# Kernel tuning notes

Hardware: AMD Instinct MI355X
Metric: run time of the kernel (lower is better)

Reference implementation:

```python
import jax, jax.numpy as jnp
import numpy as np

B, N, D, H = 16, 512, 512, 8
DK = D // H
SCALE = DK ** (-0.5)
NEG = -9.0e15
LN_EPS = 1e-5


def setup_inputs() -> dict:
    key = jax.random.key(0)
    ks = jax.random.split(key, 16)
    std = 1.0 / np.sqrt(D)
    x = jax.random.normal(ks[0], (B, N, D), jnp.float32)
    adj = jax.random.randint(ks[1], (B, N, N), 0, 2).astype(jnp.float32)
    # weights stored [in, out] (y = x @ W + b)
    def lin(k, fin, fout):
        return jax.random.normal(k, (fin, fout), jnp.float32) * (1.0 / np.sqrt(fin))
    return {
        "x": x,
        "adj": adj,
        "W_w": lin(ks[2], D, D), "W_b": jnp.zeros((D,), jnp.float32),
        "ln_g": jnp.ones((D,), jnp.float32), "ln_b": jnp.zeros((D,), jnp.float32),
        "Wq": lin(ks[3], D, D), "bq": jnp.zeros((D,), jnp.float32),
        "Wk": lin(ks[4], D, D), "bk": jnp.zeros((D,), jnp.float32),
        "Wv": lin(ks[5], D, D), "bv": jnp.zeros((D,), jnp.float32),
        "Wo": lin(ks[6], D, D), "bo": jnp.zeros((D,), jnp.float32),
        "gate_w": lin(ks[7], 2 * D, 1), "gate_b": jnp.zeros((1,), jnp.float32),
        "use_adj": 1,
    }


def _layernorm(h, g, b):
    mu = jnp.mean(h, axis=-1, keepdims=True)
    var = jnp.mean(jnp.square(h - mu), axis=-1, keepdims=True)
    return (h - mu) * jax.lax.rsqrt(var + LN_EPS) * g + b


def _forward(x, adj, W_w, W_b, ln_g, ln_b, Wq, bq, Wk, bk, Wv, bv, Wo, bo, gate_w, gate_b, use_adj):
    h = x @ W_w + W_b                      # [B,N,D]
    h = _layernorm(h, ln_g, ln_b)
    q = (h @ Wq + bq).reshape(B, N, H, DK)
    k = (h @ Wk + bk).reshape(B, N, H, DK)
    v = (h @ Wv + bv).reshape(B, N, H, DK)
    scores = jnp.einsum('bqhd,bkhd->bhqk', q * SCALE, k)   # [B,H,N,N]
    if use_adj:
        a = adj[:, None, :, :]
        scores = jnp.where(a > 0, scores, NEG) * a
    attn = jax.nn.softmax(scores, axis=-1)
    ctx = jnp.einsum('bhqk,bkhd->bqhd', attn, v).reshape(B, N, D)
    h2 = jax.nn.relu(ctx @ Wo + bo)        # dropout = identity (eval)
    coeff = jax.nn.sigmoid(jnp.concatenate([x, h2], axis=-1) @ gate_w + gate_b)  # [B,N,1]
    return coeff * x + (1.0 - coeff) * h2


def reference(x, adj, W_w, W_b, ln_g, ln_b, Wq, bq, Wk, bk, Wv, bv, Wo, bo, gate_w, gate_b, use_adj):
    return _forward(x, adj, W_w, W_b, ln_g, ln_b, Wq, bq, Wk, bk, Wv, bv, Wo, bo, gate_w, gate_b, use_adj)
```

## Files before the change

kernel.cpp:

```cpp
#include <hip/hip_runtime.h>
#include <stdint.h>


typedef __bf16 bf16_t;
typedef __bf16 bf16x8 __attribute__((ext_vector_type(8)));
typedef float  f32x4  __attribute__((ext_vector_type(4)));

#define B_   16
#define N_   512
#define D_   512
#define H_   8
#define DK_  64
#define BN_  8192
#define LOG2E 1.4426950408889634f

__device__ __forceinline__ void gl2lds16(const void* g, void* l) {
  __builtin_amdgcn_global_load_lds(
      (const __attribute__((address_space(1))) void*)g,
      (__attribute__((address_space(3))) void*)l, 16, 0, 0);
}

struct WPrep { const float* src[5]; bf16_t* dst[5]; };
__global__ __launch_bounds__(256) void k_prep(const float* __restrict__ x,
                                              bf16_t* __restrict__ xb,
                                              WPrep p) {
  __shared__ float tile[32][33];
  const int blk = blockIdx.x;
  const int t = threadIdx.x;
  if (blk < 2048) {
    const long i = ((long)blk * 256 + t) * 8;
    float4 a = *(const float4*)&x[i];
    float4 b = *(const float4*)&x[i + 4];
    bf16x8 o;
    o[0] = (bf16_t)a.x; o[1] = (bf16_t)a.y; o[2] = (bf16_t)a.z; o[3] = (bf16_t)a.w;
    o[4] = (bf16_t)b.x; o[5] = (bf16_t)b.y; o[6] = (bf16_t)b.z; o[7] = (bf16_t)b.w;
    *(bf16x8*)&xb[i] = o;
  } else {
    const int r = blk - 2048;
    const int z = r >> 8, rem = r & 255;
    const float* W = p.src[z];
    bf16_t* Wt = p.dst[z];
    const int kb = (rem & 15) * 32, nb = (rem >> 4) * 32;
    const int tx = t & 31, ty = t >> 5;
#pragma unroll
    for (int i = ty; i < 32; i += 8)
      tile[i][tx] = W[(long)(kb + i) * D_ + nb + tx];
    __syncthreads();
#pragma unroll
    for (int i = ty; i < 32; i += 8)
      Wt[(long)(nb + i) * D_ + kb + tx] = (bf16_t)tile[tx][i];
  }
}

template <int OMODE, int TN>
__global__ __launch_bounds__(256) void k_gemm128(const bf16_t* __restrict__ A,
                                                 const bf16_t* __restrict__ Bt,
                                                 const float* __restrict__ b0,
                                                 const float* __restrict__ b1,
                                                 const float* __restrict__ b2,
                                                 float s0, float s1, float s2,
                                                 void* __restrict__ outp, int ldOut,
                                                 bf16_t* __restrict__ vtp) {
  constexpr int MI = (TN == 128) ? 4 : 2;
  __shared__ bf16_t As[2][128 * 32];
  __shared__ bf16_t Bs[2][TN * 32];
  const int t = threadIdx.x;
  const int m0 = blockIdx.x * 128;
  const int n0 = blockIdx.y * TN;
  const int w = t >> 6, lane = t & 63;
  const int quad = lane >> 4, l16 = lane & 15;
  const int wm = (TN == 128) ? (w >> 1) * 64 : w * 32;
  const int wn = (TN == 128) ? (w & 1) * 64 : 0;

  const int e0 = t * 8;
  const int r0 = e0 >> 5, c0 = e0 & 31;
  const bf16_t* agp0 = A + (long)(m0 + r0) * 512 + c0;
  const bf16_t* agp1 = agp0 + (long)64 * 512;
  const bf16_t* bgp0 = Bt + (long)(n0 + r0) * 512 + c0;
  const bf16_t* bgp1 = bgp0 + (long)64 * 512;

  f32x4 acc[MI][4] = {};

  gl2lds16(agp0, &As[0][e0]);
  gl2lds16(agp1, &As[0][e0 + 2048]);
  gl2lds16(bgp0, &Bs[0][e0]);
  if (TN == 128) gl2lds16(bgp1, &Bs[0][e0 + 2048]);
  __syncthreads();

  int cur = 0;
  for (int k0 = 0; k0 < 512; k0 += 32) {
    const int nxt = cur ^ 1;
    if (k0 + 32 < 512) {
      gl2lds16(agp0 + k0 + 32, &As[nxt][e0]);
      gl2lds16(agp1 + k0 + 32, &As[nxt][e0 + 2048]);
      gl2lds16(bgp0 + k0 + 32, &Bs[nxt][e0]);
      if (TN == 128) gl2lds16(bgp1 + k0 + 32, &Bs[nxt][e0 + 2048]);
    }

    bf16x8 af[MI], bfr[4];
#pragma unroll
    for (int i = 0; i < MI; ++i)
      af[i]  = *(const bf16x8*)&As[cur][(wm + i * 16 + l16) * 32 + quad * 8];
#pragma unroll
    for (int i = 0; i < 4; ++i)
      bfr[i] = *(const bf16x8*)&Bs[cur][(wn + i * 16 + l16) * 32 + quad * 8];
#pragma unroll
    for (int mi = 0; mi < MI; ++mi)
#pragma unroll
      for (int ni = 0; ni < 4; ++ni)
        acc[mi][ni] = __builtin_amdgcn_mfma_f32_16x16x32_bf16(af[mi], bfr[ni],
                                                              acc[mi][ni], 0, 0, 0);
    __syncthreads();
    cur = nxt;
  }

  const int seg = n0 >> 9;
  const float* bias = (seg == 0) ? b0 : (seg == 1) ? b1 : b2;
  const float scale = (seg == 0) ? s0 : (seg == 1) ? s1 : s2;
#pragma unroll
  for (int ni = 0; ni < 4; ++ni) {
    const int n = n0 + wn + ni * 16 + l16;
    const float bv = bias[n & 511];
#pragma unroll
    for (int mi = 0; mi < MI; ++mi)
#pragma unroll
      for (int r = 0; r < 4; ++r) {
        const long m = m0 + wm + mi * 16 + quad * 4 + r;
        float v = (acc[mi][ni][r] + bv) * scale;
        if (OMODE == 2) v = fmaxf(v, 0.0f);
        if (OMODE == 3) {
          if (seg < 2) {
            ((bf16_t*)outp)[m * 1024 + n] = (bf16_t)v;
          } else {
            const int tok = (int)m & 511, bb = (int)(m >> 9);
            const int hh = (n >> 6) & 7, dk = n & 63;
            vtp[(((long)bb * 8 + hh) * 64 + dk) * 512 + tok] = (bf16_t)v;
          }
        } else {
          ((float*)outp)[m * ldOut + n] = v;
        }
      }
  }
}

__global__ __launch_bounds__(256) void k_layernorm(const float* __restrict__ hp,
                                                   const float* __restrict__ g,
                                                   const float* __restrict__ bb,
                                                   bf16_t* __restrict__ out) {
  const int row = blockIdx.x * 4 + (threadIdx.x >> 6);
  const int lane = threadIdx.x & 63;
  const float* hr = hp + (long)row * D_;
  float v[8];
  *(float4*)&v[0] = ((const float4*)hr)[lane * 2];
  *(float4*)&v[4] = ((const float4*)hr)[lane * 2 + 1];
  float s = 0.f;
#pragma unroll
  for (int i = 0; i < 8; ++i) s += v[i];
#pragma unroll
  for (int o = 32; o > 0; o >>= 1) s += __shfl_xor(s, o, 64);
  const float mu = s * (1.0f / 512.0f);
  float vs = 0.f;
#pragma unroll
  for (int i = 0; i < 8; ++i) { float d = v[i] - mu; vs += d * d; }
#pragma unroll
  for (int o = 32; o > 0; o >>= 1) vs += __shfl_xor(vs, o, 64);
  const float rstd = rsqrtf(vs * (1.0f / 512.0f) + 1e-5f);
  float gv[8], bv[8];
  *(float4*)&gv[0] = ((const float4*)g)[lane * 2];
  *(float4*)&gv[4] = ((const float4*)g)[lane * 2 + 1];
  *(float4*)&bv[0] = ((const float4*)bb)[lane * 2];
  *(float4*)&bv[4] = ((const float4*)bb)[lane * 2 + 1];
  bf16x8 o8;
#pragma unroll
  for (int i = 0; i < 8; ++i) o8[i] = (bf16_t)((v[i] - mu) * rstd * gv[i] + bv[i]);
  *(bf16x8*)&out[(long)row * D_ + lane * 8] = o8;
}

__global__ __launch_bounds__(256) void k_attn(const bf16_t* __restrict__ qk,
                                              const bf16_t* __restrict__ vT,
                                              const float* __restrict__ adj,
                                              const int* __restrict__ use_adj_p,
                                              bf16_t* __restrict__ ctx) {
  __shared__ bf16_t Ks[64][72];
  __shared__ bf16_t Vs[64][72];
  __shared__ bf16_t Ps[4][16][72];
  const int t = threadIdx.x;
  const int w = t >> 6, lane = t & 63;
  const int quad = lane >> 4, l16 = lane & 15;
  const int bh = blockIdx.x & 127;
  const int qt = blockIdx.x >> 7;
  const int b = bh >> 3, h = bh & 7;
  const int q0 = qt * 64;
  const int use_adj = use_adj_p[0];

  const long qoff = (long)(b * N_ + q0 + w * 16 + l16) * 1024 + h * DK_ + quad * 8;
  const bf16x8 aq0 = *(const bf16x8*)&qk[qoff];
  const bf16x8 aq1 = *(const bf16x8*)&qk[qoff + 32];

  const int sr = t >> 2, sc = (t & 3) * 16;
  const bf16_t* kbase  = qk + (long)b * N_ * 1024 + 512 + h * DK_;
  const bf16_t* vtbase = vT + (long)bh * DK_ * N_;
  const float*  abase  = adj + ((long)b * N_ + q0 + w * 16 + quad * 4) * N_;

  f32x4 accO[4] = {};
  float l_part[4] = {0.f, 0.f, 0.f, 0.f};

  for (int kt = 0; kt < 8; ++kt) {
    __syncthreads();
    {
      const bf16_t* ksrc = kbase + (long)(kt * 64 + sr) * 1024 + sc;
      *(uint4*)&Ks[sr][sc]     = *(const uint4*)ksrc;
      *(uint4*)&Ks[sr][sc + 8] = *(const uint4*)(ksrc + 8);
      const bf16_t* vsrc = vtbase + (long)sr * N_ + kt * 64 + sc;
      *(uint4*)&Vs[sr][sc]     = *(const uint4*)vsrc;
      *(uint4*)&Vs[sr][sc + 8] = *(const uint4*)(vsrc + 8);
    }
    __syncthreads();

    f32x4 s[4];
#pragma unroll
    for (int nt = 0; nt < 4; ++nt) {
      bf16x8 bk0 = *(const bf16x8*)&Ks[nt * 16 + l16][quad * 8];
      bf16x8 bk1 = *(const bf16x8*)&Ks[nt * 16 + l16][quad * 8 + 32];
      f32x4 z = {};
      z = __builtin_amdgcn_mfma_f32_16x16x32_bf16(aq0, bk0, z, 0, 0, 0);
      z = __builtin_amdgcn_mfma_f32_16x16x32_bf16(aq1, bk1, z, 0, 0, 0);
      s[nt] = z;
    }

    if (use_adj) {
#pragma unroll
      for (int nt = 0; nt < 4; ++nt)
#pragma unroll
        for (int r = 0; r < 4; ++r)
          s[nt][r] *= abase[(long)r * N_ + kt * 64 + nt * 16 + l16];
    }

#pragma unroll
    for (int nt = 0; nt < 4; ++nt)
#pragma unroll
      for (int r = 0; r < 4; ++r) {
        const float e = __builtin_amdgcn_exp2f(s[nt][r]);
        s[nt][r] = e;
        l_part[r] += e;
      }

#pragma unroll
    for (int nt = 0; nt < 4; ++nt)
#pragma unroll
      for (int r = 0; r < 4; ++r)
        Ps[w][quad * 4 + r][nt * 16 + l16] = (bf16_t)s[nt][r];
    __builtin_amdgcn_s_waitcnt(0xC07F);

    bf16x8 ap0 = *(const bf16x8*)&Ps[w][l16][quad * 8];
    bf16x8 ap1 = *(const bf16x8*)&Ps[w][l16][quad * 8 + 32];
#pragma unroll
    for (int nt = 0; nt < 4; ++nt) {
      bf16x8 bv0 = *(const bf16x8*)&Vs[nt * 16 + l16][quad * 8];
      bf16x8 bv1 = *(const bf16x8*)&Vs[nt * 16 + l16][quad * 8 + 32];
      accO[nt] = __builtin_amdgcn_mfma_f32_16x16x32_bf16(ap0, bv0, accO[nt], 0, 0, 0);
      accO[nt] = __builtin_amdgcn_mfma_f32_16x16x32_bf16(ap1, bv1, accO[nt], 0, 0, 0);
    }
  }

#pragma unroll
  for (int o = 1; o < 16; o <<= 1)
#pragma unroll
    for (int r = 0; r < 4; ++r) l_part[r] += __shfl_xor(l_part[r], o, 64);
  float inv[4];
#pragma unroll
  for (int r = 0; r < 4; ++r) inv[r] = 1.0f / l_part[r];
#pragma unroll
  for (int r = 0; r < 4; ++r) {
    const long orow = (long)(b * N_ + q0 + w * 16 + quad * 4 + r) * D_ + h * DK_;
#pragma unroll
    for (int nt = 0; nt < 4; ++nt)
      ctx[orow + nt * 16 + l16] = (bf16_t)(accO[nt][r] * inv[r]);
  }
}

__global__ __launch_bounds__(256) void k_gate(const float* __restrict__ x,
                                              const float* __restrict__ h2,
                                              const float* __restrict__ gw,
                                              const float* __restrict__ gb,
                                              float* __restrict__ outp) {
  const int row = blockIdx.x * 4 + (threadIdx.x >> 6);
  const int lane = threadIdx.x & 63;
  const long base = (long)row * D_ + lane * 8;
  float xv[8], hv[8], w0[8], w1[8];
  *(float4*)&xv[0] = *(const float4*)&x[base];
  *(float4*)&xv[4] = *(const float4*)&x[base + 4];
  *(float4*)&hv[0] = *(const float4*)&h2[base];
  *(float4*)&hv[4] = *(const float4*)&h2[base + 4];
  *(float4*)&w0[0] = *(const float4*)&gw[lane * 8];
  *(float4*)&w0[4] = *(const float4*)&gw[lane * 8 + 4];
  *(float4*)&w1[0] = *(const float4*)&gw[512 + lane * 8];
  *(float4*)&w1[4] = *(const float4*)&gw[512 + lane * 8 + 4];
  float s = 0.f;
#pragma unroll
  for (int i = 0; i < 8; ++i) s += xv[i] * w0[i] + hv[i] * w1[i];
#pragma unroll
  for (int o = 32; o > 0; o >>= 1) s += __shfl_xor(s, o, 64);
  const float z = s + gb[0];
  const float coeff = 1.0f / (1.0f + __expf(-z));
#pragma unroll
  for (int i = 0; i < 8; ++i)
    outp[base + i] = coeff * xv[i] + (1.0f - coeff) * hv[i];
}

extern "C" void kernel_launch(void* const* d_in, const int* in_sizes, int n_in,
                              void* d_out, int out_size, void* d_ws, size_t ws_size,
                              hipStream_t stream) {
  (void)in_sizes; (void)n_in; (void)out_size; (void)ws_size;
  const float* x    = (const float*)d_in[0];
  const float* adj  = (const float*)d_in[1];
  const float* W_w  = (const float*)d_in[2];
  const float* W_b  = (const float*)d_in[3];
  const float* ln_g = (const float*)d_in[4];
  const float* ln_b = (const float*)d_in[5];
  const float* Wq   = (const float*)d_in[6];
  const float* bq   = (const float*)d_in[7];
  const float* Wk   = (const float*)d_in[8];
  const float* bk   = (const float*)d_in[9];
  const float* Wv   = (const float*)d_in[10];
  const float* bv   = (const float*)d_in[11];
  const float* Wo   = (const float*)d_in[12];
  const float* bo   = (const float*)d_in[13];
  const float* gw   = (const float*)d_in[14];
  const float* gb   = (const float*)d_in[15];
  const int* use_adj = (const int*)d_in[16];

  char* ws = (char*)d_ws;
  size_t off = 0;
  auto alloc = [&](size_t bytes) -> void* {
    void* p = ws + off;
    off += (bytes + 255) & ~(size_t)255;
    return p;
  };
  bf16_t*  WtW   = (bf16_t*)alloc((size_t)D_ * D_ * 2);
  bf16_t*  WtQKV = (bf16_t*)alloc((size_t)3 * D_ * D_ * 2);
  bf16_t*  WtO   = (bf16_t*)alloc((size_t)D_ * D_ * 2);
  bf16_t*  xb    = (bf16_t*)alloc((size_t)BN_ * D_ * 2);
  float*   hPre  = (float*)alloc((size_t)BN_ * D_ * 4);
  bf16_t*  hB    = (bf16_t*)alloc((size_t)BN_ * D_ * 2);
  bf16_t*  qkB   = (bf16_t*)alloc((size_t)BN_ * 2 * D_ * 2);
  bf16_t*  vTB   = (bf16_t*)alloc((size_t)BN_ * D_ * 2);
  bf16_t*  ctxB  = (bf16_t*)alloc((size_t)BN_ * D_ * 2);
  float*   h2    = hPre;

  WPrep wp;
  wp.src[0] = W_w; wp.dst[0] = WtW;
  wp.src[1] = Wq;  wp.dst[1] = WtQKV;
  wp.src[2] = Wk;  wp.dst[2] = WtQKV + (size_t)D_ * D_;
  wp.src[3] = Wv;  wp.dst[3] = WtQKV + (size_t)2 * D_ * D_;
  wp.src[4] = Wo;  wp.dst[4] = WtO;
  k_prep<<<3328, 256, 0, stream>>>(x, xb, wp);

  dim3 gh(BN_ / 128, D_ / 64);
  dim3 gqkv(BN_ / 128, 3 * D_ / 128);
  k_gemm128<0, 64><<<gh, 256, 0, stream>>>(xb, WtW, W_b, W_b, W_b, 1.f, 1.f, 1.f,
                                           hPre, D_, nullptr);
  k_layernorm<<<BN_ / 4, 256, 0, stream>>>(hPre, ln_g, ln_b, hB);
  k_gemm128<3, 128><<<gqkv, 256, 0, stream>>>(hB, WtQKV, bq, bk, bv,
                                              0.125f * LOG2E, 1.f, 1.f, qkB, 1024, vTB);
  k_attn<<<1024, 256, 0, stream>>>(qkB, vTB, adj, use_adj, ctxB);
  k_gemm128<2, 64><<<gh, 256, 0, stream>>>(ctxB, WtO, bo, bo, bo, 1.f, 1.f, 1.f,
                                           h2, D_, nullptr);
  k_gate<<<BN_ / 4, 256, 0, stream>>>(x, h2, gw, gb, (float*)d_out);
}
```

Measured before the change: 202.7 us.

## Fuse layernorm and gate into full-row GEMM epilogues

Adds a full-row GEMM kernel in which each 512-thread block computes 32 complete output rows, so row reductions can be done in the epilogue. The first GEMM now applies layernorm directly and writes bf16, which removes the fp32 hPre round trip and the separate layernorm launch. The output-projection GEMM computes ReLU, the sigmoid gate and the blend in its epilogue, which removes the h2 buffer and the gate launch. In exchange, each block streams the whole 512x512 weight matrix through a large LDS buffer, occupancy may drop, and variance is now computed in one pass as E[x^2]-mu^2.

```diff
diff --git a/kernel.cpp b/kernel.cpp
--- a/kernel.cpp
+++ b/kernel.cpp
@@ -52,25 +52,199 @@
   }
 }
 
-template <int OMODE, int TN>
-__global__ __launch_bounds__(256) void k_gemm128(const bf16_t* __restrict__ A,
-                                                 const bf16_t* __restrict__ Bt,
-                                                 const float* __restrict__ b0,
-                                                 const float* __restrict__ b1,
-                                                 const float* __restrict__ b2,
-                                                 float s0, float s1, float s2,
-                                                 void* __restrict__ outp, int ldOut,
-                                                 bf16_t* __restrict__ vtp) {
-  constexpr int MI = (TN == 128) ? 4 : 2;
+template <int MODE>
+__global__ __launch_bounds__(512) void k_gemm_row(const bf16_t* __restrict__ A,
+                                                  const bf16_t* __restrict__ Bt,
+                                                  const float* __restrict__ bias,
+                                                  const float* __restrict__ p0,
+                                                  const float* __restrict__ p1,
+                                                  const float* __restrict__ p2,
+                                                  void* __restrict__ outp) {
+  __shared__ bf16_t As[2][32 * 32];
+  __shared__ bf16_t Bs[2][512 * 32];
+  __shared__ float red[8][32][2];
+  __shared__ float rowc[32][2];
+  const int t = threadIdx.x;
+  const int w = t >> 6, lane = t & 63;
+  const int quad = lane >> 4, l16 = lane & 15;
+  const int m0 = blockIdx.x * 32;
+  const int wn = w * 64;
+
+  const int ea = t * 8;
+  const bf16_t* agp = A + (long)(m0 + (ea >> 5)) * 512 + (ea & 31);
+  const bf16_t* bgp[4];
+  int eb[4];
+#pragma unroll
+  for (int j = 0; j < 4; ++j) {
+    eb[j] = j * 4096 + t * 8;
+    bgp[j] = Bt + (long)(eb[j] >> 5) * 512 + (eb[j] & 31);
+  }
+
+  f32x4 acc[2][4] = {};
+
+  if (t < 128) gl2lds16(agp, &As[0][ea]);
+#pragma unroll
+  for (int j = 0; j < 4; ++j) gl2lds16(bgp[j], &Bs[0][eb[j]]);
+  __syncthreads();
+
+  int cur = 0;
+  for (int k0 = 0; k0 < 512; k0 += 32) {
+    const int nxt = cur ^ 1;
+    if (k0 + 32 < 512) {
+      if (t < 128) gl2lds16(agp + k0 + 32, &As[nxt][ea]);
+#pragma unroll
+      for (int j = 0; j < 4; ++j) gl2lds16(bgp[j] + k0 + 32, &Bs[nxt][eb[j]]);
+    }
+    bf16x8 af[2], bfr[4];
+#pragma unroll
+    for (int mi = 0; mi < 2; ++mi)
+      af[mi] = *(const bf16x8*)&As[cur][(mi * 16 + l16) * 32 + quad * 8];
+#pragma unroll
+    for (int ni = 0; ni < 4; ++ni)
+      bfr[ni] = *(const bf16x8*)&Bs[cur][(wn + ni * 16 + l16) * 32 + quad * 8];
+#pragma unroll
+    for (int mi = 0; mi < 2; ++mi)
+#pragma unroll
+      for (int ni = 0; ni < 4; ++ni)
+        acc[mi][ni] = __builtin_amdgcn_mfma_f32_16x16x32_bf16(af[mi], bfr[ni],
+                                                              acc[mi][ni], 0, 0, 0);
+    __syncthreads();
+    cur = nxt;
+  }
+
+  float bv[4];
+#pragma unroll
+  for (int ni = 0; ni < 4; ++ni) bv[ni] = bias[wn + ni * 16 + l16];
+
+  if (MODE == 0) {
+#pragma unroll
+    for (int mi = 0; mi < 2; ++mi)
+#pragma unroll
+      for (int r = 0; r < 4; ++r) {
+        float s1 = 0.f, s2 = 0.f;
+#pragma unroll
+        for (int ni = 0; ni < 4; ++ni) {
+          const float v = acc[mi][ni][r] + bv[ni];
+          s1 += v; s2 += v * v;
+        }
+#pragma unroll
+        for (int o = 1; o < 16; o <<= 1) {
+          s1 += __shfl_xor(s1, o, 64);
+          s2 += __shfl_xor(s2, o, 64);
+        }
+        if (l16 == 0) {
+          const int row = mi * 16 + quad * 4 + r;
+          red[w][row][0] = s1; red[w][row][1] = s2;
+        }
+      }
+    __syncthreads();
+    if (t < 32) {
+      float S1 = 0.f, S2 = 0.f;
+#pragma unroll
+      for (int wv = 0; wv < 8; ++wv) { S1 += red[wv][t][0]; S2 += red[wv][t][1]; }
+      const float mu = S1 * (1.0f / 512.0f);
+      const float var = S2 * (1.0f / 512.0f) - mu * mu;
+      rowc[t][0] = mu;
+      rowc[t][1] = rsqrtf(var + 1e-5f);
+    }
+    __syncthreads();
+    float gv[4], b2[4];
+#pragma unroll
+    for (int ni = 0; ni < 4; ++ni) {
+      gv[ni] = p0[wn + ni * 16 + l16];
+      b2[ni] = p1[wn + ni * 16 + l16];
+    }
+#pragma unroll
+    for (int mi = 0; mi < 2; ++mi)
+#pragma unroll
+      for (int r = 0; r < 4; ++r) {
+        const int row = mi * 16 + quad * 4 + r;
+        const float mu = rowc[row][0], rs = rowc[row][1];
+#pragma unroll
+        for (int ni = 0; ni < 4; ++ni) {
+          const float v = acc[mi][ni][r] + bv[ni];
+          ((bf16_t*)outp)[(long)(m0 + row) * 512 + wn + ni * 16 + l16] =
+              (bf16_t)((v - mu) * rs * gv[ni] + b2[ni]);
+        }
+      }
+  } else {
+    float g0[4], g1[4];
+#pragma unroll
+    for (int ni = 0; ni < 4; ++ni) {
+      g0[ni] = p1[wn + ni * 16 + l16];
+      g1[ni] = p1[512 + wn + ni * 16 + l16];
+    }
+    float xr[2][4][4];
+#pragma unroll
+    for (int mi = 0; mi < 2; ++mi)
+#pragma unroll
+      for (int r = 0; r < 4; ++r) {
+        const int row = mi * 16 + quad * 4 + r;
+#pragma unroll
+        for (int ni = 0; ni < 4; ++ni)
+          xr[mi][ni][r] = p0[(long)(m0 + row) * 512 + wn + ni * 16 + l16];
+      }
+#pragma unroll
+    for (int mi = 0; mi < 2; ++mi)
+#pragma unroll
+      for (int r = 0; r < 4; ++r) {
+        float px = 0.f, ph = 0.f;
+#pragma unroll
+        for (int ni = 0; ni < 4; ++ni) {
+          const float h2 = fmaxf(acc[mi][ni][r] + bv[ni], 0.0f);
+          px += xr[mi][ni][r] * g0[ni];
+          ph += h2 * g1[ni];
+        }
+#pragma unroll
+        for (int o = 1; o < 16; o <<= 1) {
+          px += __shfl_xor(px, o, 64);
+          ph += __shfl_xor(ph, o, 64);
+        }
+        if (l16 == 0) {
+          const int row = mi * 16 + quad * 4 + r;
+          red[w][row][0] = px; red[w][row][1] = ph;
+        }
+      }
+    __syncthreads();
+    if (t < 32) {
+      float z = p2[0];
+#pragma unroll
+      for (int wv = 0; wv < 8; ++wv) z += red[wv][t][0] + red[wv][t][1];
+      rowc[t][0] = 1.0f / (1.0f + __expf(-z));
+    }
+    __syncthreads();
+#pragma unroll
+    for (int mi = 0; mi < 2; ++mi)
+#pragma unroll
+      for (int r = 0; r < 4; ++r) {
+        const int row = mi * 16 + quad * 4 + r;
+        const float c = rowc[row][0];
+#pragma unroll
+        for (int ni = 0; ni < 4; ++ni) {
+          const float h2 = fmaxf(acc[mi][ni][r] + bv[ni], 0.0f);
+          ((float*)outp)[(long)(m0 + row) * 512 + wn + ni * 16 + l16] =
+              c * xr[mi][ni][r] + (1.0f - c) * h2;
+        }
+      }
+  }
+}
+
+__global__ __launch_bounds__(256) void k_gemm_qkv(const bf16_t* __restrict__ A,
+                                                  const bf16_t* __restrict__ Bt,
+                                                  const float* __restrict__ b0,
+                                                  const float* __restrict__ b1,
+                                                  const float* __restrict__ b2,
+                                                  float s0,
+                                                  bf16_t* __restrict__ outp,
+                                                  bf16_t* __restrict__ vtp) {
   __shared__ bf16_t As[2][128 * 32];
-  __shared__ bf16_t Bs[2][TN * 32];
+  __shared__ bf16_t Bs[2][128 * 32];
   const int t = threadIdx.x;
   const int m0 = blockIdx.x * 128;
-  const int n0 = blockIdx.y * TN;
+  const int n0 = blockIdx.y * 128;
   const int w = t >> 6, lane = t & 63;
   const int quad = lane >> 4, l16 = lane & 15;
-  const int wm = (TN == 128) ? (w >> 1) * 64 : w * 32;
-  const int wn = (TN == 128) ? (w & 1) * 64 : 0;
+  const int wm = (w >> 1) * 64, wn = (w & 1) * 64;
 
   const int e0 = t * 8;
   const int r0 = e0 >> 5, c0 = e0 & 31;
@@ -79,12 +253,12 @@
   const bf16_t* bgp0 = Bt + (long)(n0 + r0) * 512 + c0;
   const bf16_t* bgp1 = bgp0 + (long)64 * 512;
 
-  f32x4 acc[MI][4] = {};
+  f32x4 acc[4][4] = {};
 
   gl2lds16(agp0, &As[0][e0]);
   gl2lds16(agp1, &As[0][e0 + 2048]);
   gl2lds16(bgp0, &Bs[0][e0]);
-  if (TN == 128) gl2lds16(bgp1, &Bs[0][e0 + 2048]);
+  gl2lds16(bgp1, &Bs[0][e0 + 2048]);
   __syncthreads();
 
   int cur = 0;
@@ -94,18 +268,16 @@
       gl2lds16(agp0 + k0 + 32, &As[nxt][e0]);
       gl2lds16(agp1 + k0 + 32, &As[nxt][e0 + 2048]);
       gl2lds16(bgp0 + k0 + 32, &Bs[nxt][e0]);
-      if (TN == 128) gl2lds16(bgp1 + k0 + 32, &Bs[nxt][e0 + 2048]);
-    }
-
-    bf16x8 af[MI], bfr[4];
-#pragma unroll
-    for (int i = 0; i < MI; ++i)
+      gl2lds16(bgp1 + k0 + 32, &Bs[nxt][e0 + 2048]);
+    }
+    bf16x8 af[4], bfr[4];
+#pragma unroll
+    for (int i = 0; i < 4; ++i) {
       af[i]  = *(const bf16x8*)&As[cur][(wm + i * 16 + l16) * 32 + quad * 8];
-#pragma unroll
-    for (int i = 0; i < 4; ++i)
       bfr[i] = *(const bf16x8*)&Bs[cur][(wn + i * 16 + l16) * 32 + quad * 8];
-#pragma unroll
-    for (int mi = 0; mi < MI; ++mi)
+    }
+#pragma unroll
+    for (int mi = 0; mi < 4; ++mi)
 #pragma unroll
       for (int ni = 0; ni < 4; ++ni)
         acc[mi][ni] = __builtin_amdgcn_mfma_f32_16x16x32_bf16(af[mi], bfr[ni],
@@ -116,64 +288,26 @@
 
   const int seg = n0 >> 9;
   const float* bias = (seg == 0) ? b0 : (seg == 1) ? b1 : b2;
-  const float scale = (seg == 0) ? s0 : (seg == 1) ? s1 : s2;
+  const float scale = (seg == 0) ? s0 : 1.0f;
 #pragma unroll
   for (int ni = 0; ni < 4; ++ni) {
     const int n = n0 + wn + ni * 16 + l16;
-    const float bv = bias[n & 511];
-#pragma unroll
-    for (int mi = 0; mi < MI; ++mi)
+    const float bvv = bias[n & 511];
+#pragma unroll
+    for (int mi = 0; mi < 4; ++mi)
 #pragma unroll
       for (int r = 0; r < 4; ++r) {
         const long m = m0 + wm + mi * 16 + quad * 4 + r;
-        float v = (acc[mi][ni][r] + bv) * scale;
-        if (OMODE == 2) v = fmaxf(v, 0.0f);
-        if (OMODE == 3) {
-          if (seg < 2) {
-            ((bf16_t*)outp)[m * 1024 + n] = (bf16_t)v;
-          } else {
-            const int tok = (int)m & 511, bb = (int)(m >> 9);
-            const int hh = (n >> 6) & 7, dk = n & 63;
-            vtp[(((long)bb * 8 + hh) * 64 + dk) * 512 + tok] = (bf16_t)v;
-          }
+        const float v = (acc[mi][ni][r] + bvv) * scale;
+        if (seg < 2) {
+          outp[m * 1024 + n] = (bf16_t)v;
         } else {
-          ((float*)outp)[m * ldOut + n] = v;
-        }
-      }
-  }
-}
-
-__global__ __launch_bounds__(256) void k_layernorm(const float* __restrict__ hp,
-                                                   const float* __restrict__ g,
-                                                   const float* __restrict__ bb,
-                                                   bf16_t* __restrict__ out) {
-  const int row = blockIdx.x * 4 + (threadIdx.x >> 6);
-  const int lane = threadIdx.x & 63;
-  const float* hr = hp + (long)row * D_;
-  float v[8];
-  *(float4*)&v[0] = ((const float4*)hr)[lane * 2];
-  *(float4*)&v[4] = ((const float4*)hr)[lane * 2 + 1];
-  float s = 0.f;
-#pragma unroll
-  for (int i = 0; i < 8; ++i) s += v[i];
-#pragma unroll
-  for (int o = 32; o > 0; o >>= 1) s += __shfl_xor(s, o, 64);
-  const float mu = s * (1.0f / 512.0f);
-  float vs = 0.f;
-#pragma unroll
-  for (int i = 0; i < 8; ++i) { float d = v[i] - mu; vs += d * d; }
-#pragma unroll
-  for (int o = 32; o > 0; o >>= 1) vs += __shfl_xor(vs, o, 64);
-  const float rstd = rsqrtf(vs * (1.0f / 512.0f) + 1e-5f);
-  float gv[8], bv[8];
-  *(float4*)&gv[0] = ((const float4*)g)[lane * 2];
-  *(float4*)&gv[4] = ((const float4*)g)[lane * 2 + 1];
-  *(float4*)&bv[0] = ((const float4*)bb)[lane * 2];
-  *(float4*)&bv[4] = ((const float4*)bb)[lane * 2 + 1];
-  bf16x8 o8;
-#pragma unroll
-  for (int i = 0; i < 8; ++i) o8[i] = (bf16_t)((v[i] - mu) * rstd * gv[i] + bv[i]);
-  *(bf16x8*)&out[(long)row * D_ + lane * 8] = o8;
+          const int tok = (int)m & 511, bb = (int)(m >> 9);
+          const int hh = (n >> 6) & 7, dk = n & 63;
+          vtp[(((long)bb * 8 + hh) * 64 + dk) * 512 + tok] = (bf16_t)v;
+        }
+      }
+  }
 }
 
 __global__ __launch_bounds__(256) void k_attn(const bf16_t* __restrict__ qk,
@@ -277,35 +411,6 @@
     for (int nt = 0; nt < 4; ++nt)
       ctx[orow + nt * 16 + l16] = (bf16_t)(accO[nt][r] * inv[r]);
   }
-}
-
-__global__ __launch_bounds__(256) void k_gate(const float* __restrict__ x,
-                                              const float* __restrict__ h2,
-                                              const float* __restrict__ gw,
-                                              const float* __restrict__ gb,
-                                              float* __restrict__ outp) {
-  const int row = blockIdx.x * 4 + (threadIdx.x >> 6);
-  const int lane = threadIdx.x & 63;
-  const long base = (long)row * D_ + lane * 8;
-  float xv[8], hv[8], w0[8], w1[8];
-  *(float4*)&xv[0] = *(const float4*)&x[base];
-  *(float4*)&xv[4] = *(const float4*)&x[base + 4];
-  *(float4*)&hv[0] = *(const float4*)&h2[base];
-  *(float4*)&hv[4] = *(const float4*)&h2[base + 4];
-  *(float4*)&w0[0] = *(const float4*)&gw[lane * 8];
-  *(float4*)&w0[4] = *(const float4*)&gw[lane * 8 + 4];
-  *(float4*)&w1[0] = *(const float4*)&gw[512 + lane * 8];
-  *(float4*)&w1[4] = *(const float4*)&gw[512 + lane * 8 + 4];
-  float s = 0.f;
-#pragma unroll
-  for (int i = 0; i < 8; ++i) s += xv[i] * w0[i] + hv[i] * w1[i];
-#pragma unroll
-  for (int o = 32; o > 0; o >>= 1) s += __shfl_xor(s, o, 64);
-  const float z = s + gb[0];
-  const float coeff = 1.0f / (1.0f + __expf(-z));
-#pragma unroll
-  for (int i = 0; i < 8; ++i)
-    outp[base + i] = coeff * xv[i] + (1.0f - coeff) * hv[i];
 }
 
 extern "C" void kernel_launch(void* const* d_in, const int* in_sizes, int n_in,
@@ -341,12 +446,10 @@
   bf16_t*  WtQKV = (bf16_t*)alloc((size_t)3 * D_ * D_ * 2);
   bf16_t*  WtO   = (bf16_t*)alloc((size_t)D_ * D_ * 2);
   bf16_t*  xb    = (bf16_t*)alloc((size_t)BN_ * D_ * 2);
-  float*   hPre  = (float*)alloc((size_t)BN_ * D_ * 4);
   bf16_t*  hB    = (bf16_t*)alloc((size_t)BN_ * D_ * 2);
   bf16_t*  qkB   = (bf16_t*)alloc((size_t)BN_ * 2 * D_ * 2);
   bf16_t*  vTB   = (bf16_t*)alloc((size_t)BN_ * D_ * 2);
   bf16_t*  ctxB  = (bf16_t*)alloc((size_t)BN_ * D_ * 2);
-  float*   h2    = hPre;
 
   WPrep wp;
   wp.src[0] = W_w; wp.dst[0] = WtW;
@@ -356,15 +459,10 @@
   wp.src[4] = Wo;  wp.dst[4] = WtO;
   k_prep<<<3328, 256, 0, stream>>>(x, xb, wp);
 
-  dim3 gh(BN_ / 128, D_ / 64);
+  k_gemm_row<0><<<BN_ / 32, 512, 0, stream>>>(xb, WtW, W_b, ln_g, ln_b, nullptr, hB);
   dim3 gqkv(BN_ / 128, 3 * D_ / 128);
-  k_gemm128<0, 64><<<gh, 256, 0, stream>>>(xb, WtW, W_b, W_b, W_b, 1.f, 1.f, 1.f,
-                                           hPre, D_, nullptr);
-  k_layernorm<<<BN_ / 4, 256, 0, stream>>>(hPre, ln_g, ln_b, hB);
-  k_gemm128<3, 128><<<gqkv, 256, 0, stream>>>(hB, WtQKV, bq, bk, bv,
-                                              0.125f * LOG2E, 1.f, 1.f, qkB, 1024, vTB);
+  k_gemm_qkv<<<gqkv, 256, 0, stream>>>(hB, WtQKV, bq, bk, bv,
+                                       0.125f * LOG2E, qkB, vTB);
   k_attn<<<1024, 256, 0, stream>>>(qkB, vTB, adj, use_adj, ctxB);
-  k_gemm128<2, 64><<<gh, 256, 0, stream>>>(ctxB, WtO, bo, bo, bo, 1.f, 1.f, 1.f,
-                                           h2, D_, nullptr);
-  k_gate<<<BN_ / 4, 256, 0, stream>>>(x, h2, gw, gb, (float*)d_out);
-}
+  k_gemm_row<1><<<BN_ / 32, 512, 0, stream>>>(ctxB, WtO, bo, x, gw, gb, d_out);
+}
```

Result: no change. 204.6 us (+0.9%).
